# Kernel tuning notes

Measured on AMD Instinct MI355X. Metric: run time of the kernel, lower is better.

The kernel has to match this reference:

```python
import jax, jax.numpy as jnp
import numpy as np

# static config (matches init_kwargs)
B, T, D = 4, 1024, 512
H, G = 8, 2
HD = D // H            # 64
REP = H // G           # 4
CHUNK = 64
LC = 2 * CHUNK         # left_context = context_chunk_number * chunk_size = 128
MAXPOS = CHUNK + LC    # 192
NLAYER = 4
EPS = 1e-4
NEG = -50000.0


def _ln(x, w, b):
    m = x.mean(-1, keepdims=True)
    v = ((x - m) ** 2).mean(-1, keepdims=True)
    return (x - m) / jnp.sqrt(v + EPS) * w + b


def _chunk_mask(mask_length):
    # get_mask_vector(CHUNK, mask_length, LC)
    corr = (mask_length + CHUNK - 1) // CHUNK * CHUNK
    row = jnp.arange(corr)[:, None]
    col = jnp.arange(corr + LC)[None, :]
    start = (row // CHUNK) * CHUNK
    cm = (col >= start) & (col < start + CHUNK + LC)
    cm = cm[:mask_length, LC:LC + mask_length]
    return jnp.where(cm, 0.0, -jnp.inf)


def _cut_masks(mask, lens):
    # _cut_masks_with_len_vector
    Lm = mask.shape[0]
    lim = (lens + LC)[:, None]                      # [B,1]
    inb = jnp.arange(Lm)[None, :] < lim             # [B,Lm]
    valid = inb[:, :, None] & inb[:, None, :]       # [B,Lm,Lm]
    return jnp.where(valid, mask[None], NEG)


def _attn(xp, wq, wk, wv, wo, rel_tab, mask):
    # GQASelfAttentionRelPos forward. xp:[B,Tp,D], mask:[B,Tp,Tp]
    Bb, Tp, _ = xp.shape
    scale = 1.0 / jnp.sqrt(jnp.float32(HD))
    q = (xp @ wq.T).reshape(Bb, Tp, H, HD) * scale
    k = jnp.repeat((xp @ wk.T).reshape(Bb, Tp, G, HD), REP, axis=2)
    v = jnp.repeat((xp @ wv.T).reshape(Bb, Tp, G, HD), REP, axis=2)
    scores = jnp.einsum('bqhd,bkhd->bhqk', q, k)
    r = jnp.arange(Tp)
    dist = jnp.clip(r[None, :] - r[:, None], -(MAXPOS - 1), MAXPOS - 1) + MAXPOS - 1
    rel = rel_tab[dist]                              # [Tp,Tp,HD], row=query
    scores = scores + jnp.einsum('bqhd,kqd->bhqk', q, rel)  # matches 'bhd,thd->bht'
    scores = scores + mask[:, None]                  # broadcast over heads
    p = jax.nn.softmax(scores, axis=-1)
    out = jnp.einsum('bhqk,bkhd->bqhd', p, v).reshape(Bb, Tp, D)
    return out @ wo.T


def _conv(x, pw1, dw, pw2):
    # Conformer-style ConvModule(d_model, kernel=9): pointwise->GLU->depthwise->SiLU->pointwise
    h = x @ pw1.T                                   # [B,T,2D]
    a, g = jnp.split(h, 2, axis=-1)
    h = a * jax.nn.sigmoid(g)                       # GLU
    h = jnp.transpose(h, (0, 2, 1))                 # [B,D,T]
    h = jax.lax.conv_general_dilated(h, dw[:, None, :], (1,), [(4, 4)],
                                     dimension_numbers=('NCH', 'OIH', 'NCH'),
                                     feature_group_count=D)
    h = jax.nn.silu(h)
    h = jnp.transpose(h, (0, 2, 1))
    return h @ pw2.T


def _ffn(x, w1, w2):
    # SwiGLUFFN(factor=2)
    h = x @ w1.T
    a, b = jnp.split(h, 2, axis=-1)
    return (jax.nn.silu(a) * b) @ w2.T


def setup_inputs() -> dict:
    key = jax.random.key(0)
    ks = iter(jax.random.split(key, 40))
    s = 0.02
    def rn(shape):
        return jax.random.normal(next(ks), shape, jnp.float32) * s
    L = NLAYER
    return {
        'x': jax.random.normal(next(ks), (B, T, D), jnp.float32),
        'audio_len': jax.random.randint(next(ks), (B,), 1, T + 1),
        'ln1_w': jnp.ones((L, D), jnp.float32), 'ln1_b': jnp.zeros((L, D), jnp.float32),
        'wq': rn((L, D, D)), 'wk': rn((L, G * HD, D)), 'wv': rn((L, G * HD, D)), 'wo': rn((L, D, D)),
        'rel_emb': rn((L, 2 * MAXPOS - 1, HD)),
        'ln2_w': jnp.ones((L, D), jnp.float32), 'ln2_b': jnp.zeros((L, D), jnp.float32),
        'conv_pw1': rn((L, 2 * D, D)), 'conv_dw': rn((L, D, 9)), 'conv_pw2': rn((L, D, D)),
        'ln3_w': jnp.ones((L, D), jnp.float32), 'ln3_b': jnp.zeros((L, D), jnp.float32),
        'ffn_w1': rn((L, 4 * D, D)), 'ffn_w2': rn((L, D, 2 * D)),
    }


def reference(x, audio_len, ln1_w, ln1_b, wq, wk, wv, wo, rel_emb,
              ln2_w, ln2_b, conv_pw1, conv_dw, conv_pw2,
              ln3_w, ln3_b, ffn_w1, ffn_w2):
    mask = _cut_masks(_chunk_mask(T + LC), audio_len)   # [B,Tp,Tp]
    for i in range(NLAYER):
        x = _ln(x, ln1_w[i], ln1_b[i])
        xp = jnp.pad(x, ((0, 0), (LC, 0), (0, 0)))
        x = x + _attn(xp, wq[i], wk[i], wv[i], wo[i], rel_emb[i], mask)[:, LC:]
        x = _ln(x, ln2_w[i], ln2_b[i])
        x = x + _conv(x, conv_pw1[i], conv_dw[i], conv_pw2[i])
        x = _ln(x, ln3_w[i], ln3_b[i])
        x = x + _ffn(x, ffn_w1[i], ffn_w2[i])
    return x
```

## Files before the change

### kernel.cpp

```cpp
#include <hip/hip_runtime.h>
#include <hip/hip_bf16.h>

typedef __hip_bfloat16 bf16;
typedef unsigned short ushort_t;
typedef unsigned int uint_t;
typedef __attribute__((ext_vector_type(8))) short short8;
typedef __attribute__((ext_vector_type(4))) float floatx4;

__device__ __forceinline__ float b2f(bf16 x) { return __bfloat162float(x); }
__device__ __forceinline__ ushort_t f2us(float f) { bf16 h = __float2bfloat16(f); return *(ushort_t*)&h; }
__device__ __forceinline__ float us2f(ushort_t u) { return __uint_as_float(((uint_t)u) << 16); }

constexpr int Bc = 4, Tc = 1024, Dc = 512, Hc = 8, HDc = 64;
constexpr int LCc = 128, MPc = 192;
constexpr float EPSc = 1e-4f;
constexpr int NBT = Bc * Tc;
constexpr long NE = (long)NBT * Dc;
constexpr float NEGB = -1e30f;
constexpr int PSTRIDE = 8704;

__device__ __forceinline__ float wload(const void* p, long i, int f32) {
  return f32 ? ((const float*)p)[i] : b2f(((const bf16*)p)[i]);
}

__device__ __forceinline__ void stage_swz(const ushort_t* __restrict__ G, int rowStride,
                                          int rowBase, int k0, ushort_t* L, int nChunk, int t) {
#pragma unroll
  for (int i = t; i < nChunk; i += 256) {
    int r = i >> 3;
    int cs = (i & 7) ^ (r & 7);
    const ushort_t* gp = G + (long)(rowBase + r) * rowStride + k0 + cs * 8;
    __builtin_amdgcn_global_load_lds(
        (const __attribute__((address_space(1))) void*)gp,
        (__attribute__((address_space(3))) void*)&L[(i & ~63) * 8], 16, 0, 0);
  }
}

__global__ void k_detect(const void* __restrict__ x, int* __restrict__ flag) {
  __shared__ int s[256];
  int t = threadIdx.x;
  const unsigned short* u = (const unsigned short*)x;
  int bad = 0;
  for (int j = t; j < 2048; j += 256) {
    int e = (u[j] >> 7) & 0xFF;
    if (e == 0xFF || e > 0x8F || (e != 0 && e < 0x6F)) bad++;
  }
  s[t] = bad;
  __syncthreads();
  for (int off = 128; off > 0; off >>= 1) { if (t < off) s[t] += s[t + off]; __syncthreads(); }
  if (t == 0) flag[0] = (s[0] > 16) ? 1 : 0;
}

__global__ void k_in(const void* __restrict__ in, float* __restrict__ out, int n,
                     const int* __restrict__ flag) {
  int i = blockIdx.x * 256 + threadIdx.x;
  if (i < n) out[i] = wload(in, i, flag[0]);
}
__global__ void k_out(const float* __restrict__ in, void* __restrict__ out, int n,
                      const int* __restrict__ flag) {
  int i = blockIdx.x * 256 + threadIdx.x;
  if (i >= n) return;
  if (flag[0]) ((float*)out)[i] = in[i];
  else         ((bf16*)out)[i] = __float2bfloat16(in[i]);
}
__global__ void k_w2b(const void* __restrict__ src, ushort_t* __restrict__ dst, int n,
                      const int* __restrict__ flag) {
  int i = blockIdx.x * 256 + threadIdx.x;
  if (i < n) dst[i] = f2us(wload(src, i, flag[0]));
}
__global__ void k_w2bT(const void* __restrict__ src, ushort_t* __restrict__ dst,
                       const int* __restrict__ flag) {
  int i = blockIdx.x * 256 + threadIdx.x;
  if (i >= 18432) return;
  int l = i / 4608, rem = i - l * 4608;
  int j = rem >> 9, d = rem & 511;
  dst[i] = f2us(wload(src, (long)l * 4608 + d * 9 + j, flag[0]));
}

__global__ __launch_bounds__(256) void k_ln(const float* __restrict__ x,
    const void* __restrict__ w, const void* __restrict__ bb, long woff,
    float* __restrict__ o, ushort_t* __restrict__ oA, const int* __restrict__ flag) {
  int f32 = flag[0];
  int row = blockIdx.x;
  int t = threadIdx.x;
  int lane = t & 63, wv = t >> 6;
  float2 v = ((const float2*)(x + (long)row * Dc))[t];
  float s = v.x + v.y;
#pragma unroll
  for (int o2 = 1; o2 < 64; o2 <<= 1) s += __shfl_xor(s, o2, 64);
  __shared__ float ws[8];
  if (lane == 0) ws[wv] = s;
  __syncthreads();
  float mean = (ws[0] + ws[1] + ws[2] + ws[3]) * (1.0f / Dc);
  float dx = v.x - mean, dy = v.y - mean;
  float s2 = dx * dx + dy * dy;
#pragma unroll
  for (int o2 = 1; o2 < 64; o2 <<= 1) s2 += __shfl_xor(s2, o2, 64);
  if (lane == 0) ws[4 + wv] = s2;
  __syncthreads();
  float inv = 1.0f / sqrtf((ws[4] + ws[5] + ws[6] + ws[7]) * (1.0f / Dc) + EPSc);
  float v0 = dx * inv * wload(w, woff + 2 * t, f32)     + wload(bb, woff + 2 * t, f32);
  float v1 = dy * inv * wload(w, woff + 2 * t + 1, f32) + wload(bb, woff + 2 * t + 1, f32);
  float2 ov; ov.x = v0; ov.y = v1;
  ((float2*)(o + (long)row * Dc))[t] = ov;
  ((uint_t*)(oA + (long)row * Dc))[t] = (uint_t)f2us(v0) | ((uint_t)f2us(v1) << 16);
}

template<int BM, int BN, bool OBF>
__global__ __launch_bounds__(256) void k_gemm_b(const ushort_t* __restrict__ A, int lda,
    const ushort_t* __restrict__ W, void* __restrict__ C, int ldc,
    const float* __restrict__ addend, float alpha, int K) {
  constexpr int WGM = BM / 64;
  constexpr int WGN = 4 / WGM;
  constexpr int WN = BN / WGN;
  constexpr int NJ = WN / 16;
  __shared__ ushort_t As[BM * 64];
  __shared__ ushort_t Ws[BN * 64];
  int t = threadIdx.x;
  int m0 = blockIdx.y * BM, n0 = blockIdx.x * BN;
  int lane = t & 63, wv = t >> 6;
  int l15 = lane & 15, quad = lane >> 4;
  int wrow = (WGM == 2) ? (wv >> 1) * 64 : 0;
  int wcol = (WGM == 2) ? (wv & 1) * WN : wv * WN;
  floatx4 acc[4][NJ];
#pragma unroll
  for (int i = 0; i < 4; ++i)
#pragma unroll
    for (int j = 0; j < NJ; ++j) acc[i][j] = 0;
  for (int k0 = 0; k0 < K; k0 += 64) {
    stage_swz(A, lda, m0, k0, As, BM * 8, t);
    stage_swz(W, K,  n0, k0, Ws, BN * 8, t);
    __syncthreads();
#pragma unroll
    for (int half = 0; half < 2; ++half) {
      int sw = ((half * 4 + quad) ^ (l15 & 7)) << 3;
      short8 af[4], bfr[NJ];
#pragma unroll
      for (int i = 0; i < 4; ++i) af[i] = *(short8*)&As[(wrow + i * 16 + l15) * 64 + sw];
#pragma unroll
      for (int j = 0; j < NJ; ++j) bfr[j] = *(short8*)&Ws[(wcol + j * 16 + l15) * 64 + sw];
#pragma unroll
      for (int i = 0; i < 4; ++i)
#pragma unroll
        for (int j = 0; j < NJ; ++j)
          acc[i][j] = __builtin_amdgcn_mfma_f32_16x16x32_bf16(af[i], bfr[j], acc[i][j], 0, 0, 0);
    }
    __syncthreads();
  }
#pragma unroll
  for (int i = 0; i < 4; ++i) {
#pragma unroll
    for (int j = 0; j < NJ; ++j) {
#pragma unroll
      for (int rg = 0; rg < 4; ++rg) {
        int m = m0 + wrow + i * 16 + quad * 4 + rg;
        int n = n0 + wcol + j * 16 + l15;
        float v = alpha * acc[i][j][rg];
        if (addend) v += addend[(long)m * ldc + n];
        if (OBF) ((ushort_t*)C)[(long)m * ldc + n] = f2us(v);
        else     ((float*)C)[(long)m * ldc + n] = v;
      }
    }
  }
}

__global__ __launch_bounds__(256, 3) void k_attn(const ushort_t* __restrict__ q,
    const ushort_t* __restrict__ kb, const ushort_t* __restrict__ vb,
    const ushort_t* __restrict__ relL, const int* __restrict__ alen,
    ushort_t* __restrict__ out, char* __restrict__ part) {
  int bx = blockIdx.x;
  int h = blockIdx.y, b = blockIdx.z;
  int len = alen[b];
  int inv, qt, grp;
  if (bx < 16) { inv = 0; qt = bx; grp = 0; }
  else         { inv = 1; qt = (bx - 16) & 15; grp = (bx - 16) >> 4; }
  int q0 = qt * 64;
  if (inv) { if (q0 + 64 <= len) return; }
  else     { if (q0 >= len) return; }
  int nvalid = min(len - q0, 64);
  int g = h >> 2;
  __shared__ __align__(16) ushort_t UQB[8704];
  __shared__ __align__(16) ushort_t Ks[64 * 64];
  __shared__ __align__(16) ushort_t Vt[64 * 72];
  __shared__ __align__(16) ushort_t Ps[64 * 64];
  __shared__ __align__(16) float fML[128];
  ushort_t* Qs = UQB;
  ushort_t* B2t = UQB;
  int t = threadIdx.x;
  int lane = t & 63, w = t >> 6;
  int l15 = lane & 15, quad = lane >> 4;
  int qw = w * 16;
  {
    int qi = t >> 2, du = (t & 3) * 16;
    const ushort_t* src = q + ((long)(b * Tc + q0 + qi)) * Dc + h * 64 + du;
    *(uint4*)&Qs[qi * 72 + du] = *(const uint4*)(src);
    *(uint4*)&Qs[qi * 72 + du + 8] = *(const uint4*)(src + 8);
  }
  const int koB = inv ? -128 : (q0 - 128);
  const int KSTEP = inv ? 4 : 1;
  const int nIt = inv ? ((grp < 2) ? 5 : 4) : 3;
  uint4 kr0, kr1, vr0, vr1;
  int kj = t >> 2, du = (t & 3) * 16, c0 = du >> 3;
  auto LOADKV = [&](int kt2) {
    int ko = koB + kt2 * 64 + kj;
    if (ko >= 0) {
      long basek = ((long)(b * Tc + ko)) * 128 + g * 64 + du;
      kr0 = *(const uint4*)(kb + basek);
      kr1 = *(const uint4*)(kb + basek + 8);
      vr0 = *(const uint4*)(vb + basek);
      vr1 = *(const uint4*)(vb + basek + 8);
    } else {
      uint4 z = {0, 0, 0, 0};
      kr0 = z; kr1 = z; vr0 = z; vr1 = z;
    }
  };
  LOADKV(grp);
  float m_ = NEGB, l_ = 0.f;
  floatx4 acc[4];
#pragma unroll
  for (int j = 0; j < 4; ++j) acc[j] = 0;
  __syncthreads();
  short8 aq0 = *(short8*)&Qs[(qw + l15) * 72 + quad * 8];
  short8 aq1 = *(short8*)&Qs[(qw + l15) * 72 + 32 + quad * 8];
  float rv_lo = 0.f, rv_hi = 0.f;
  if (inv) {
    int er = (l15 == 1) ? 382 : 0;
    short8 be0 = *(const short8*)(relL + (long)er * 64 + quad * 8);
    short8 be1 = *(const short8*)(relL + (long)er * 64 + 32 + quad * 8);
    floatx4 ec = {0.f, 0.f, 0.f, 0.f};
    ec = __builtin_amdgcn_mfma_f32_16x16x32_bf16(be0, aq0, ec, 0, 0, 0);
    ec = __builtin_amdgcn_mfma_f32_16x16x32_bf16(be1, aq1, ec, 0, 0, 0);
    rv_lo = __shfl(ec[0], l15, 64);
    rv_hi = __shfl(ec[1], l15, 64);
  }
  int sw7 = l15 & 7;
  for (int it = 0; it < nIt; ++it) {
    int kt = inv ? (grp + it * KSTEP) : it;
    int ko0 = koB + kt * 64;
    int t0 = q0 - ko0 + 191;
    bool far_hi = (q0 - ko0 - 63) >= 191;
    bool far_lo = (q0 + 63 - ko0) <= -191;
    bool near = !far_hi && !far_lo;
    int cb = min(max(t0 - 63, 0), 255);
    __syncthreads();
    {
      *(uint4*)&Ks[kj * 64 + ((c0 ^ (kj & 7)) << 3)] = kr0;
      *(uint4*)&Ks[kj * 64 + (((c0 + 1) ^ (kj & 7)) << 3)] = kr1;
      uint_t wds[8] = {vr0.x, vr0.y, vr0.z, vr0.w, vr1.x, vr1.y, vr1.z, vr1.w};
#pragma unroll
      for (int u = 0; u < 8; ++u) {
        Vt[(du + 2 * u) * 72 + kj] = (ushort_t)(wds[u] & 0xffff);
        Vt[(du + 2 * u + 1) * 72 + kj] = (ushort_t)(wds[u] >> 16);
      }
    }
    if (near) {
      __builtin_amdgcn_s_setprio(1);
#pragma unroll
      for (int p = 0; p < 2; ++p) {
        short8 rw0[4], rw1[4];
#pragma unroll
        for (int j = 0; j < 4; ++j) {
          long wr = cb + (p * 4 + j) * 16 + l15;
          rw0[j] = *(const short8*)(relL + wr * 64 + quad * 8);
          rw1[j] = *(const short8*)(relL + wr * 64 + 32 + quad * 8);
        }
#pragma unroll
        for (int j = 0; j < 4; ++j) {
          floatx4 z = {0.f, 0.f, 0.f, 0.f};
          z = __builtin_amdgcn_mfma_f32_16x16x32_bf16(rw0[j], aq0, z, 0, 0, 0);
          z = __builtin_amdgcn_mfma_f32_16x16x32_bf16(rw1[j], aq1, z, 0, 0, 0);
#pragma unroll
          for (int rg = 0; rg < 4; ++rg) {
            int cpr = (p * 4 + j) * 16 + quad * 4 + rg;
            B2t[cpr * 68 + qw + l15] = f2us(z[rg]);
          }
        }
      }
      __builtin_amdgcn_s_setprio(0);
    }
    __syncthreads();
    if (it + 1 < nIt) LOADKV(kt + KSTEP);
    floatx4 s[4];
    __builtin_amdgcn_s_setprio(1);
#pragma unroll
    for (int nt = 0; nt < 4; ++nt) {
      short8 ak0 = *(short8*)&Ks[(nt * 16 + l15) * 64 + ((quad ^ sw7) << 3)];
      short8 ak1 = *(short8*)&Ks[(nt * 16 + l15) * 64 + (((4 + quad) ^ sw7) << 3)];
      floatx4 z = {0.f, 0.f, 0.f, 0.f};
      z = __builtin_amdgcn_mfma_f32_16x16x32_bf16(ak0, aq0, z, 0, 0, 0);
      z = __builtin_amdgcn_mfma_f32_16x16x32_bf16(ak1, aq1, z, 0, 0, 0);
      s[nt] = z;
    }
    __builtin_amdgcn_s_setprio(0);
    if (near) {
#pragma unroll
      for (int nt = 0; nt < 4; ++nt)
#pragma unroll
        for (int rg = 0; rg < 4; ++rg) {
          int c = t0 + qw + l15 - (nt * 16 + quad * 4 + rg);
          c = min(max(c, 0), 382);
          s[nt][rg] += us2f(B2t[(c - cb) * 68 + qw + l15]);
        }
    } else {
      float rv = far_hi ? rv_hi : rv_lo;
#pragma unroll
      for (int nt = 0; nt < 4; ++nt)
#pragma unroll
        for (int rg = 0; rg < 4; ++rg) s[nt][rg] += rv;
    }
    if (!inv) {
#pragma unroll
      for (int nt = 0; nt < 4; ++nt)
#pragma unroll
        for (int rg = 0; rg < 4; ++rg) {
          int ko = ko0 + nt * 16 + quad * 4 + rg;
          if (ko >= len) s[nt][rg] = NEGB;
        }
    }
    float mx = s[0][0];
#pragma unroll
    for (int nt = 0; nt < 4; ++nt)
#pragma unroll
      for (int rg = 0; rg < 4; ++rg) mx = fmaxf(mx, s[nt][rg]);
    mx = fmaxf(mx, __shfl_xor(mx, 16, 64));
    mx = fmaxf(mx, __shfl_xor(mx, 32, 64));
    float mn = fmaxf(m_, mx);
    float al = __expf(m_ - mn);
    float ps = 0.f;
#pragma unroll
    for (int nt = 0; nt < 4; ++nt)
#pragma unroll
      for (int rg = 0; rg < 4; ++rg) {
        float p = __expf(s[nt][rg] - mn);
        s[nt][rg] = p;
        ps += p;
      }
    ps += __shfl_xor(ps, 16, 64);
    ps += __shfl_xor(ps, 32, 64);
    l_ = l_ * al + ps;
    m_ = mn;
    if (quad == 0) fML[qw + l15] = al;
#pragma unroll
    for (int nt = 0; nt < 4; ++nt)
#pragma unroll
      for (int pr = 0; pr < 2; ++pr) {
        uint_t pk = (uint_t)f2us(s[nt][2 * pr]) | ((uint_t)f2us(s[nt][2 * pr + 1]) << 16);
        int e = nt * 16 + quad * 4 + pr * 2;
        *(uint_t*)&Ps[(qw + l15) * 64 + (((e >> 3) ^ sw7) << 3) + (e & 7)] = pk;
      }
    floatx4 av = *(floatx4*)&fML[qw + quad * 4];
#pragma unroll
    for (int j = 0; j < 4; ++j)
#pragma unroll
      for (int rg = 0; rg < 4; ++rg) acc[j][rg] *= av[rg];
    short8 ap0 = *(short8*)&Ps[(qw + l15) * 64 + ((quad ^ sw7) << 3)];
    short8 ap1 = *(short8*)&Ps[(qw + l15) * 64 + (((4 + quad) ^ sw7) << 3)];
    __builtin_amdgcn_s_setprio(1);
#pragma unroll
    for (int j = 0; j < 4; ++j) {
      short8 bv0 = *(short8*)&Vt[(j * 16 + l15) * 72 + quad * 8];
      short8 bv1 = *(short8*)&Vt[(j * 16 + l15) * 72 + 32 + quad * 8];
      acc[j] = __builtin_amdgcn_mfma_f32_16x16x32_bf16(ap0, bv0, acc[j], 0, 0, 0);
      acc[j] = __builtin_amdgcn_mfma_f32_16x16x32_bf16(ap1, bv1, acc[j], 0, 0, 0);
    }
    __builtin_amdgcn_s_setprio(0);
  }
  if (inv) {
    char* pp = part + (long)((((b * 8 + h) * 16 + qt) * 4 + grp)) * PSTRIDE;
    ushort_t* Cp = (ushort_t*)pp;
    float* mp = (float*)(pp + 8192);
#pragma unroll
    for (int j = 0; j < 4; ++j)
#pragma unroll
      for (int rg = 0; rg < 4; ++rg)
        Cp[(qw + quad * 4 + rg) * 64 + j * 16 + l15] = f2us(acc[j][rg]);
    if (quad == 0) { mp[qw + l15] = m_; mp[64 + qw + l15] = l_; }
  } else {
    if (quad == 0) fML[64 + qw + l15] = l_;
    floatx4 lv = *(floatx4*)&fML[64 + qw + quad * 4];
#pragma unroll
    for (int rg = 0; rg < 4; ++rg) {
      int R = qw + quad * 4 + rg;
      if (R < nvalid) {
        float invL = 1.0f / lv[rg];
#pragma unroll
        for (int j = 0; j < 4; ++j)
          out[((long)(b * Tc + q0 + R)) * Dc + h * 64 + j * 16 + l15] = f2us(acc[j][rg] * invL);
      }
    }
  }
}

__global__ __launch_bounds__(256) void k_comb(const char* __restrict__ part,
    const int* __restrict__ alen, ushort_t* __restrict__ out) {
  int qt = blockIdx.x, h = blockIdx.y, b = blockIdx.z;
  int len = alen[b];
  int q0 = qt * 64;
  if (q0 + 64 <= len) return;
  int nskip = max(len - q0, 0);
  int t = threadIdx.x;
  int d = t & 63, r0 = (t >> 6) * 16;
  const char* pb = part + (long)(((b * 8 + h) * 16 + qt) * 4) * PSTRIDE;
#pragma unroll 4
  for (int i = 0; i < 16; ++i) {
    int r = r0 + i;
    if (r < nskip) continue;
    float mg[4], lg[4], M = NEGB;
#pragma unroll
    for (int g2 = 0; g2 < 4; ++g2) {
      const float* mp = (const float*)(pb + g2 * PSTRIDE + 8192);
      mg[g2] = mp[r];
      lg[g2] = mp[64 + r];
      M = fmaxf(M, mg[g2]);
    }
    float L = 0.f, wgt[4];
#pragma unroll
    for (int g2 = 0; g2 < 4; ++g2) { wgt[g2] = __expf(mg[g2] - M); L += lg[g2] * wgt[g2]; }
    float v = 0.f;
#pragma unroll
    for (int g2 = 0; g2 < 4; ++g2)
      v += us2f(((const ushort_t*)(pb + g2 * PSTRIDE))[r * 64 + d]) * wgt[g2];
    out[((long)(b * Tc + q0 + r)) * Dc + h * 64 + d] = f2us(v / L);
  }
}

__global__ void k_glu(ushort_t* __restrict__ h, int n8) {
  int i = blockIdx.x * 256 + threadIdx.x;
  if (i >= n8) return;
  long r = i >> 6;
  int j8 = (i & 63) << 3;
  short8 a8 = *(short8*)&h[r * 1024 + j8];
  short8 g8 = *(short8*)&h[r * 1024 + 512 + j8];
  short8 o8;
#pragma unroll
  for (int e = 0; e < 8; ++e) {
    float a = us2f((ushort_t)a8[e]), g = us2f((ushort_t)g8[e]);
    o8[e] = (short)f2us(a * (1.0f / (1.0f + __expf(-g))));
  }
  *(short8*)&h[r * 1024 + j8] = o8;
}
__global__ void k_swiglu(ushort_t* __restrict__ h, int n8) {
  int i = blockIdx.x * 256 + threadIdx.x;
  if (i >= n8) return;
  long r = i >> 7;
  int j8 = (i & 127) << 3;
  short8 a8 = *(short8*)&h[r * 2048 + j8];
  short8 b8 = *(short8*)&h[r * 2048 + 1024 + j8];
  short8 o8;
#pragma unroll
  for (int e = 0; e < 8; ++e) {
    float a = us2f((ushort_t)a8[e]), bb = us2f((ushort_t)b8[e]);
    o8[e] = (short)f2us((a / (1.0f + __expf(-a))) * bb);
  }
  *(short8*)&h[r * 2048 + j8] = o8;
}
__global__ void k_dwconv(const ushort_t* __restrict__ in, const ushort_t* __restrict__ dwT,
                         ushort_t* __restrict__ out, int n8) {
  int i = blockIdx.x * 256 + threadIdx.x;
  if (i >= n8) return;
  int row = i >> 6;
  int d8 = (i & 63) << 3;
  int t = row & (Tc - 1);
  int b = row >> 10;
  float acc[8] = {0, 0, 0, 0, 0, 0, 0, 0};
#pragma unroll
  for (int j = 0; j < 9; ++j) {
    int tt = t + j - 4;
    if (tt < 0 || tt >= Tc) continue;
    short8 vv = *(const short8*)&in[((long)(b * Tc + tt) << 10) + d8];
    short8 dv = *(const short8*)&dwT[j * 512 + d8];
#pragma unroll
    for (int e = 0; e < 8; ++e)
      acc[e] += us2f((ushort_t)vv[e]) * us2f((ushort_t)dv[e]);
  }
  short8 o8;
#pragma unroll
  for (int e = 0; e < 8; ++e)
    o8[e] = (short)f2us(acc[e] * (1.0f / (1.0f + __expf(-acc[e]))));
  *(short8*)&out[(long)row * 512 + d8] = o8;
}

extern "C" void kernel_launch(void* const* d_in, const int* in_sizes, int n_in,
                              void* d_out, int out_size, void* d_ws, size_t ws_size,
                              hipStream_t stream) {
  const void* x_in = d_in[0];
  const int*  alen = (const int*)d_in[1];
  const void* ln1w = d_in[2];
  const void* ln1b = d_in[3];
  const void* wq   = d_in[4];
  const void* wk   = d_in[5];
  const void* wv   = d_in[6];
  const void* wo   = d_in[7];
  const void* rel  = d_in[8];
  const void* ln2w = d_in[9];
  const void* ln2b = d_in[10];
  const void* pw1  = d_in[11];
  const void* dwv  = d_in[12];
  const void* pw2  = d_in[13];
  const void* ln3w = d_in[14];
  const void* ln3b = d_in[15];
  const void* w1   = d_in[16];
  const void* w2   = d_in[17];

  char* base = (char*)d_ws;
  int*      flag = (int*)base;
  float*    xf   = (float*)(base + 256);
  float*    lnb  = (float*)(base + 256 + 8388608);
  ushort_t* lnA  = (ushort_t*)(base + 16777472);
  ushort_t* wbf  = (ushort_t*)(base + 20971776);
  char*     U    = base + 45321984;
  ushort_t* qb = (ushort_t*)U;
  ushort_t* kb = (ushort_t*)(U + 4194304);
  ushort_t* vb = (ushort_t*)(U + 5242880);
  ushort_t* ab = (ushort_t*)(U + 6291456);
  char*     partA = U + 10485760;
  ushort_t* big = (ushort_t*)U;
  ushort_t* cb  = (ushort_t*)(U + 16777216);
  size_t REQ = 45321984 + 16777216 + 4194304;
  size_t REQ2 = 45321984 + 35651584;
  if (REQ2 > REQ) REQ = REQ2;
  if (ws_size < REQ) return;

  ushort_t* wqB  = wbf + 0;
  ushort_t* wkB  = wbf + 1048576;
  ushort_t* wvB  = wbf + 1310720;
  ushort_t* woB  = wbf + 1572864;
  ushort_t* relB = wbf + 2621440;
  ushort_t* pw1B = wbf + 2719488;
  ushort_t* dwB  = wbf + 4816640;
  ushort_t* pw2B = wbf + 4835072;
  ushort_t* w1B  = wbf + 5883648;
  ushort_t* w2B  = wbf + 10077952;

  k_detect<<<1, 256, 0, stream>>>(x_in, flag);
  k_in<<<(int)((NE + 255) / 256), 256, 0, stream>>>(x_in, xf, (int)NE, flag);
  k_w2b<<<4096, 256, 0, stream>>>(wq,  wqB,  1048576, flag);
  k_w2b<<<1024, 256, 0, stream>>>(wk,  wkB,  262144, flag);
  k_w2b<<<1024, 256, 0, stream>>>(wv,  wvB,  262144, flag);
  k_w2b<<<4096, 256, 0, stream>>>(wo,  woB,  1048576, flag);
  k_w2b<<<383,  256, 0, stream>>>(rel, relB, 98048, flag);
  k_w2b<<<8192, 256, 0, stream>>>(pw1, pw1B, 2097152, flag);
  k_w2bT<<<72,  256, 0, stream>>>(dwv, dwB, flag);
  k_w2b<<<4096, 256, 0, stream>>>(pw2, pw2B, 1048576, flag);
  k_w2b<<<16384,256, 0, stream>>>(w1,  w1B,  4194304, flag);
  k_w2b<<<8192, 256, 0, stream>>>(w2,  w2B,  2097152, flag);

  for (int i = 0; i < 4; ++i) {
    long oLN = (long)i * Dc;
    k_ln<<<NBT, 256, 0, stream>>>(xf, ln1w, ln1b, oLN, lnb, lnA, flag);
    k_gemm_b<64, 128, true><<<dim3(4, 64), 256, 0, stream>>>(lnA, Dc, wqB + (long)i * 262144, qb, Dc, nullptr, 0.125f, 512);
    k_gemm_b<64, 64, true><<<dim3(2, 64), 256, 0, stream>>>(lnA, Dc, wkB + (long)i * 65536, kb, 128, nullptr, 1.0f, 512);
    k_gemm_b<64, 64, true><<<dim3(2, 64), 256, 0, stream>>>(lnA, Dc, wvB + (long)i * 65536, vb, 128, nullptr, 1.0f, 512);
    k_attn<<<dim3(80, 8, 4), 256, 0, stream>>>(qb, kb, vb, relB + (long)i * 24512, alen, ab, partA);
    k_comb<<<dim3(16, 8, 4), 256, 0, stream>>>(partA, alen, ab);
    k_gemm_b<64, 128, false><<<dim3(4, 64), 256, 0, stream>>>(ab, Dc, woB + (long)i * 262144, xf, Dc, lnb, 1.0f, 512);

    k_ln<<<NBT, 256, 0, stream>>>(xf, ln2w, ln2b, oLN, lnb, lnA, flag);
    k_gemm_b<128, 128, true><<<dim3(8, 32), 256, 0, stream>>>(lnA, Dc, pw1B + (long)i * 524288, big, 1024, nullptr, 1.0f, 512);
    k_glu<<<NBT * 512 / 8 / 256, 256, 0, stream>>>(big, NBT * 512 / 8);
    k_dwconv<<<NBT * 512 / 8 / 256, 256, 0, stream>>>(big, dwB + (long)i * 4608, cb, NBT * 512 / 8);
    k_gemm_b<64, 128, false><<<dim3(4, 64), 256, 0, stream>>>(cb, Dc, pw2B + (long)i * 262144, xf, Dc, lnb, 1.0f, 512);

    k_ln<<<NBT, 256, 0, stream>>>(xf, ln3w, ln3b, oLN, lnb, lnA, flag);
    k_gemm_b<128, 128, true><<<dim3(16, 32), 256, 0, stream>>>(lnA, Dc, w1B + (long)i * 1048576, big, 2048, nullptr, 1.0f, 512);
    k_swiglu<<<NBT * 1024 / 8 / 256, 256, 0, stream>>>(big, NBT * 1024 / 8);
    k_gemm_b<64, 128, false><<<dim3(4, 64), 256, 0, stream>>>(big, 2048, w2B + (long)i * 524288, xf, Dc, lnb, 1.0f, 1024);
  }

  k_out<<<(int)((NE + 255) / 256), 256, 0, stream>>>(xf, d_out, (int)NE, flag);
}
```

Before: 1.028 ms.

## Fuse GLU/SwiGLU into gate GEMMs, merge K/V projection, batch weight conversion

Adds a dual-accumulator GEMM that computes the value and gate halves of the conv pointwise and FFN up-projections together and applies GLU or SwiGLU in the epilogue. This removes the separate elementwise kernels and halves the intermediate written to memory. K and V projections now run as one GEMM writing an interleaved KV buffer, which attention reads with new offsets. The ten weight-conversion launches become a single kernel. The cost is a larger shared-memory footprint and more registers in the gate GEMM, which may lower occupancy.

New measurement: 945.6 us. 8.1% less time.

```diff
diff --git a/kernel.cpp b/kernel.cpp
--- a/kernel.cpp
+++ b/kernel.cpp
@@ -63,18 +63,42 @@
   if (flag[0]) ((float*)out)[i] = in[i];
   else         ((bf16*)out)[i] = __float2bfloat16(in[i]);
 }
-__global__ void k_w2b(const void* __restrict__ src, ushort_t* __restrict__ dst, int n,
-                      const int* __restrict__ flag) {
-  int i = blockIdx.x * 256 + threadIdx.x;
-  if (i < n) dst[i] = f2us(wload(src, i, flag[0]));
-}
-__global__ void k_w2bT(const void* __restrict__ src, ushort_t* __restrict__ dst,
-                       const int* __restrict__ flag) {
-  int i = blockIdx.x * 256 + threadIdx.x;
-  if (i >= 18432) return;
-  int l = i / 4608, rem = i - l * 4608;
-  int j = rem >> 9, d = rem & 511;
-  dst[i] = f2us(wload(src, (long)l * 4608 + d * 9 + j, flag[0]));
+
+__global__ void k_w2all(const void* wq, const void* wk, const void* wv, const void* wo,
+                        const void* rel, const void* pw1, const void* dwv, const void* pw2,
+                        const void* w1, const void* w2,
+                        ushort_t* __restrict__ wbf, const int* __restrict__ flag) {
+  int f32 = flag[0];
+  long i = (long)blockIdx.x * 256 + threadIdx.x;
+  if (i >= 12175104L) return;
+  float v;
+  if (i < 1048576) {
+    v = wload(wq, i, f32);
+  } else if (i < 1572864) {
+    long r2 = i - 1048576;
+    long l = r2 / 131072, rem = r2 - l * 131072;
+    int r = (int)(rem >> 9), c = (int)(rem & 511);
+    if (r < 128) v = wload(wk, l * 65536 + (long)r * 512 + c, f32);
+    else         v = wload(wv, l * 65536 + (long)(r - 128) * 512 + c, f32);
+  } else if (i < 2621440) {
+    v = wload(wo, i - 1572864, f32);
+  } else if (i < 2719488) {
+    v = wload(rel, i - 2621440, f32);
+  } else if (i < 4816640) {
+    v = wload(pw1, i - 2719488, f32);
+  } else if (i < 4835072) {
+    long r2 = i - 4816640;
+    long l = r2 / 4608, rem = r2 - l * 4608;
+    int j = (int)(rem >> 9), d = (int)(rem & 511);
+    v = wload(dwv, l * 4608 + (long)d * 9 + j, f32);
+  } else if (i < 5883648) {
+    v = wload(pw2, i - 4835072, f32);
+  } else if (i < 10077952) {
+    v = wload(w1, i - 5883648, f32);
+  } else {
+    v = wload(w2, i - 10077952, f32);
+  }
+  wbf[i] = f2us(v);
 }
 
 __global__ __launch_bounds__(256) void k_ln(const float* __restrict__ x,
@@ -164,8 +188,69 @@
   }
 }
 
+template<int MODE>
+__global__ __launch_bounds__(256) void k_gemm_gate(const ushort_t* __restrict__ A, int lda,
+    const ushort_t* __restrict__ Wa, const ushort_t* __restrict__ Wg,
+    ushort_t* __restrict__ C, int ldc, int K) {
+  __shared__ ushort_t As[64 * 64];
+  __shared__ ushort_t Wsa[128 * 64];
+  __shared__ ushort_t Wsg[128 * 64];
+  int t = threadIdx.x;
+  int m0 = blockIdx.y * 64, n0 = blockIdx.x * 128;
+  int lane = t & 63, wv = t >> 6;
+  int l15 = lane & 15, quad = lane >> 4;
+  int wcol = wv * 32;
+  floatx4 acca[4][2], accg[4][2];
+#pragma unroll
+  for (int i = 0; i < 4; ++i)
+#pragma unroll
+    for (int j = 0; j < 2; ++j) { acca[i][j] = 0; accg[i][j] = 0; }
+  for (int k0 = 0; k0 < K; k0 += 64) {
+    stage_swz(A, lda, m0, k0, As, 512, t);
+    stage_swz(Wa, K, n0, k0, Wsa, 1024, t);
+    stage_swz(Wg, K, n0, k0, Wsg, 1024, t);
+    __syncthreads();
+#pragma unroll
+    for (int half = 0; half < 2; ++half) {
+      int sw = ((half * 4 + quad) ^ (l15 & 7)) << 3;
+      short8 af[4], ba[2], bg[2];
+#pragma unroll
+      for (int i = 0; i < 4; ++i) af[i] = *(short8*)&As[(i * 16 + l15) * 64 + sw];
+#pragma unroll
+      for (int j = 0; j < 2; ++j) {
+        ba[j] = *(short8*)&Wsa[(wcol + j * 16 + l15) * 64 + sw];
+        bg[j] = *(short8*)&Wsg[(wcol + j * 16 + l15) * 64 + sw];
+      }
+#pragma unroll
+      for (int i = 0; i < 4; ++i)
+#pragma unroll
+        for (int j = 0; j < 2; ++j) {
+          acca[i][j] = __builtin_amdgcn_mfma_f32_16x16x32_bf16(af[i], ba[j], acca[i][j], 0, 0, 0);
+          accg[i][j] = __builtin_amdgcn_mfma_f32_16x16x32_bf16(af[i], bg[j], accg[i][j], 0, 0, 0);
+        }
+    }
+    __syncthreads();
+  }
+#pragma unroll
+  for (int i = 0; i < 4; ++i) {
+#pragma unroll
+    for (int j = 0; j < 2; ++j) {
+#pragma unroll
+      for (int rg = 0; rg < 4; ++rg) {
+        int m = m0 + i * 16 + quad * 4 + rg;
+        int n = n0 + wcol + j * 16 + l15;
+        float a = acca[i][j][rg], g = accg[i][j][rg];
+        float v;
+        if (MODE == 0) v = a * (1.0f / (1.0f + __expf(-g)));
+        else           v = (a / (1.0f + __expf(-a))) * g;
+        C[(long)m * ldc + n] = f2us(v);
+      }
+    }
+  }
+}
+
 __global__ __launch_bounds__(256, 3) void k_attn(const ushort_t* __restrict__ q,
-    const ushort_t* __restrict__ kb, const ushort_t* __restrict__ vb,
+    const ushort_t* __restrict__ kvb,
     const ushort_t* __restrict__ relL, const int* __restrict__ alen,
     ushort_t* __restrict__ out, char* __restrict__ part) {
   int bx = blockIdx.x;
@@ -204,11 +289,11 @@
   auto LOADKV = [&](int kt2) {
     int ko = koB + kt2 * 64 + kj;
     if (ko >= 0) {
-      long basek = ((long)(b * Tc + ko)) * 128 + g * 64 + du;
-      kr0 = *(const uint4*)(kb + basek);
-      kr1 = *(const uint4*)(kb + basek + 8);
-      vr0 = *(const uint4*)(vb + basek);
-      vr1 = *(const uint4*)(vb + basek + 8);
+      long basek = ((long)(b * Tc + ko)) * 256 + g * 64 + du;
+      kr0 = *(const uint4*)(kvb + basek);
+      kr1 = *(const uint4*)(kvb + basek + 8);
+      vr0 = *(const uint4*)(kvb + basek + 128);
+      vr1 = *(const uint4*)(kvb + basek + 136);
     } else {
       uint4 z = {0, 0, 0, 0};
       kr0 = z; kr1 = z; vr0 = z; vr1 = z;
@@ -424,36 +509,6 @@
   }
 }
 
-__global__ void k_glu(ushort_t* __restrict__ h, int n8) {
-  int i = blockIdx.x * 256 + threadIdx.x;
-  if (i >= n8) return;
-  long r = i >> 6;
-  int j8 = (i & 63) << 3;
-  short8 a8 = *(short8*)&h[r * 1024 + j8];
-  short8 g8 = *(short8*)&h[r * 1024 + 512 + j8];
-  short8 o8;
-#pragma unroll
-  for (int e = 0; e < 8; ++e) {
-    float a = us2f((ushort_t)a8[e]), g = us2f((ushort_t)g8[e]);
-    o8[e] = (short)f2us(a * (1.0f / (1.0f + __expf(-g))));
-  }
-  *(short8*)&h[r * 1024 + j8] = o8;
-}
-__global__ void k_swiglu(ushort_t* __restrict__ h, int n8) {
-  int i = blockIdx.x * 256 + threadIdx.x;
-  if (i >= n8) return;
-  long r = i >> 7;
-  int j8 = (i & 127) << 3;
-  short8 a8 = *(short8*)&h[r * 2048 + j8];
-  short8 b8 = *(short8*)&h[r * 2048 + 1024 + j8];
-  short8 o8;
-#pragma unroll
-  for (int e = 0; e < 8; ++e) {
-    float a = us2f((ushort_t)a8[e]), bb = us2f((ushort_t)b8[e]);
-    o8[e] = (short)f2us((a / (1.0f + __expf(-a))) * bb);
-  }
-  *(short8*)&h[r * 2048 + j8] = o8;
-}
 __global__ void k_dwconv(const ushort_t* __restrict__ in, const ushort_t* __restrict__ dwT,
                          ushort_t* __restrict__ out, int n8) {
   int i = blockIdx.x * 256 + threadIdx.x;
@@ -467,7 +522,7 @@
   for (int j = 0; j < 9; ++j) {
     int tt = t + j - 4;
     if (tt < 0 || tt >= Tc) continue;
-    short8 vv = *(const short8*)&in[((long)(b * Tc + tt) << 10) + d8];
+    short8 vv = *(const short8*)&in[((long)(b * Tc + tt) << 9) + d8];
     short8 dv = *(const short8*)&dwT[j * 512 + d8];
 #pragma unroll
     for (int e = 0; e < 8; ++e)
@@ -509,10 +564,9 @@
   ushort_t* lnA  = (ushort_t*)(base + 16777472);
   ushort_t* wbf  = (ushort_t*)(base + 20971776);
   char*     U    = base + 45321984;
-  ushort_t* qb = (ushort_t*)U;
-  ushort_t* kb = (ushort_t*)(U + 4194304);
-  ushort_t* vb = (ushort_t*)(U + 5242880);
-  ushort_t* ab = (ushort_t*)(U + 6291456);
+  ushort_t* qb  = (ushort_t*)U;
+  ushort_t* kvb = (ushort_t*)(U + 4194304);
+  ushort_t* ab  = (ushort_t*)(U + 6291456);
   char*     partA = U + 10485760;
   ushort_t* big = (ushort_t*)U;
   ushort_t* cb  = (ushort_t*)(U + 16777216);
@@ -521,50 +575,39 @@
   if (REQ2 > REQ) REQ = REQ2;
   if (ws_size < REQ) return;
 
-  ushort_t* wqB  = wbf + 0;
-  ushort_t* wkB  = wbf + 1048576;
-  ushort_t* wvB  = wbf + 1310720;
-  ushort_t* woB  = wbf + 1572864;
-  ushort_t* relB = wbf + 2621440;
-  ushort_t* pw1B = wbf + 2719488;
-  ushort_t* dwB  = wbf + 4816640;
-  ushort_t* pw2B = wbf + 4835072;
-  ushort_t* w1B  = wbf + 5883648;
-  ushort_t* w2B  = wbf + 10077952;
+  ushort_t* wqB   = wbf + 0;
+  ushort_t* wkvB  = wbf + 1048576;
+  ushort_t* woB   = wbf + 1572864;
+  ushort_t* relB  = wbf + 2621440;
+  ushort_t* pw1B  = wbf + 2719488;
+  ushort_t* dwB   = wbf + 4816640;
+  ushort_t* pw2B  = wbf + 4835072;
+  ushort_t* w1B   = wbf + 5883648;
+  ushort_t* w2B   = wbf + 10077952;
 
   k_detect<<<1, 256, 0, stream>>>(x_in, flag);
   k_in<<<(int)((NE + 255) / 256), 256, 0, stream>>>(x_in, xf, (int)NE, flag);
-  k_w2b<<<4096, 256, 0, stream>>>(wq,  wqB,  1048576, flag);
-  k_w2b<<<1024, 256, 0, stream>>>(wk,  wkB,  262144, flag);
-  k_w2b<<<1024, 256, 0, stream>>>(wv,  wvB,  262144, flag);
-  k_w2b<<<4096, 256, 0, stream>>>(wo,  woB,  1048576, flag);
-  k_w2b<<<383,  256, 0, stream>>>(rel, relB, 98048, flag);
-  k_w2b<<<8192, 256, 0, stream>>>(pw1, pw1B, 2097152, flag);
-  k_w2bT<<<72,  256, 0, stream>>>(dwv, dwB, flag);
-  k_w2b<<<4096, 256, 0, stream>>>(pw2, pw2B, 1048576, flag);
-  k_w2b<<<16384,256, 0, stream>>>(w1,  w1B,  4194304, flag);
-  k_w2b<<<8192, 256, 0, stream>>>(w2,  w2B,  2097152, flag);
+  k_w2all<<<47559, 256, 0, stream>>>(wq, wk, wv, wo, rel, pw1, dwv, pw2, w1, w2, wbf, flag);
 
   for (int i = 0; i < 4; ++i) {
     long oLN = (long)i * Dc;
     k_ln<<<NBT, 256, 0, stream>>>(xf, ln1w, ln1b, oLN, lnb, lnA, flag);
     k_gemm_b<64, 128, true><<<dim3(4, 64), 256, 0, stream>>>(lnA, Dc, wqB + (long)i * 262144, qb, Dc, nullptr, 0.125f, 512);
-    k_gemm_b<64, 64, true><<<dim3(2, 64), 256, 0, stream>>>(lnA, Dc, wkB + (long)i * 65536, kb, 128, nullptr, 1.0f, 512);
-    k_gemm_b<64, 64, true><<<dim3(2, 64), 256, 0, stream>>>(lnA, Dc, wvB + (long)i * 65536, vb, 128, nullptr, 1.0f, 512);
-    k_attn<<<dim3(80, 8, 4), 256, 0, stream>>>(qb, kb, vb, relB + (long)i * 24512, alen, ab, partA);
+    k_gemm_b<64, 128, true><<<dim3(2, 64), 256, 0, stream>>>(lnA, Dc, wkvB + (long)i * 131072, kvb, 256, nullptr, 1.0f, 512);
+    k_attn<<<dim3(80, 8, 4), 256, 0, stream>>>(qb, kvb, relB + (long)i * 24512, alen, ab, partA);
     k_comb<<<dim3(16, 8, 4), 256, 0, stream>>>(partA, alen, ab);
     k_gemm_b<64, 128, false><<<dim3(4, 64), 256, 0, stream>>>(ab, Dc, woB + (long)i * 262144, xf, Dc, lnb, 1.0f, 512);
 
     k_ln<<<NBT, 256, 0, stream>>>(xf, ln2w, ln2b, oLN, lnb, lnA, flag);
-    k_gemm_b<128, 128, true><<<dim3(8, 32), 256, 0, stream>>>(lnA, Dc, pw1B + (long)i * 524288, big, 1024, nullptr, 1.0f, 512);
-    k_glu<<<NBT * 512 / 8 / 256, 256, 0, stream>>>(big, NBT * 512 / 8);
+    k_gemm_gate<0><<<dim3(4, 64), 256, 0, stream>>>(lnA, Dc, pw1B + (long)i * 524288,
+        pw1B + (long)i * 524288 + 262144, big, 512, 512);
     k_dwconv<<<NBT * 512 / 8 / 256, 256, 0, stream>>>(big, dwB + (long)i * 4608, cb, NBT * 512 / 8);
     k_gemm_b<64, 128, false><<<dim3(4, 64), 256, 0, stream>>>(cb, Dc, pw2B + (long)i * 262144, xf, Dc, lnb, 1.0f, 512);
 
     k_ln<<<NBT, 256, 0, stream>>>(xf, ln3w, ln3b, oLN, lnb, lnA, flag);
-    k_gemm_b<128, 128, true><<<dim3(16, 32), 256, 0, stream>>>(lnA, Dc, w1B + (long)i * 1048576, big, 2048, nullptr, 1.0f, 512);
-    k_swiglu<<<NBT * 1024 / 8 / 256, 256, 0, stream>>>(big, NBT * 1024 / 8);
-    k_gemm_b<64, 128, false><<<dim3(4, 64), 256, 0, stream>>>(big, 2048, w2B + (long)i * 524288, xf, Dc, lnb, 1.0f, 1024);
+    k_gemm_gate<1><<<dim3(8, 64), 256, 0, stream>>>(lnA, Dc, w1B + (long)i * 1048576,
+        w1B + (long)i * 1048576 + 524288, big, 1024, 512);
+    k_gemm_b<64, 128, false><<<dim3(4, 64), 256, 0, stream>>>(big, 1024, w2B + (long)i * 524288, xf, Dc, lnb, 1.0f, 1024);
   }
 
   k_out<<<(int)((NE + 255) / 256), 256, 0, stream>>>(xf, d_out, (int)NE, flag);
```
